# Optimization experiments

Hardware: AMD Instinct MI355X
Metric: run time of the kernel (lower is better)

The kernel has to match this reference:

```python
import jax, jax.numpy as jnp
import numpy as np

K = 9                # snake kernel size
CENTER = K // 2
EXT = 1.0            # extend_scope
EPS = 1e-5           # GroupNorm eps (torch default)


def conv2d(x, w, b, stride, padding):
    out = jax.lax.conv_general_dilated(
        x, w, window_strides=stride, padding=padding,
        dimension_numbers=("NCHW", "OIHW", "NCHW"))
    return out + b[None, :, None, None]


def group_norm(x, gamma, beta, groups):
    B, C, H, W = x.shape
    xg = x.reshape(B, groups, C // groups, H, W)
    mu = xg.mean(axis=(2, 3, 4), keepdims=True)
    var = xg.var(axis=(2, 3, 4), keepdims=True)
    xn = ((xg - mu) / jnp.sqrt(var + EPS)).reshape(B, C, H, W)
    return xn * gamma[None, :, None, None] + beta[None, :, None, None]


def setup_inputs() -> dict:
    key = jax.random.key(0)
    ks = jax.random.split(key, 6)
    B, Cin, Cout, H, W = 4, 64, 64, 128, 128
    x = jax.random.normal(ks[0], (B, Cin, H, W), jnp.float32)
    w_off = jax.random.normal(ks[1], (2 * K, Cin, 3, 3), jnp.float32) * 0.05
    b_off = jax.random.normal(ks[2], (2 * K,), jnp.float32) * 0.01
    g_gn_off = jnp.ones((2 * K,), jnp.float32)
    b_gn_off = jnp.zeros((2 * K,), jnp.float32)
    w_dsc = jax.random.normal(ks[3], (Cout, Cin, K, 1), jnp.float32) * 0.05
    b_dsc = jax.random.normal(ks[4], (Cout,), jnp.float32) * 0.01
    g_gn = jnp.ones((Cout,), jnp.float32)
    b_gn = jnp.zeros((Cout,), jnp.float32)
    return {"x": x, "w_off": w_off, "b_off": b_off,
            "g_gn_off": g_gn_off, "b_gn_off": b_gn_off,
            "w_dsc": w_dsc, "b_dsc": b_dsc, "g_gn": g_gn, "b_gn": b_gn}


def reference(x, w_off, b_off, g_gn_off, b_gn_off, w_dsc, b_dsc, g_gn, b_gn):
    B, Cin, H, W = x.shape
    # offset branch: conv3x3 -> GN(K groups over 2K chans) -> tanh
    off = conv2d(x, w_off, b_off, (1, 1), "SAME")
    off = jnp.tanh(group_norm(off, g_gn_off, b_gn_off, K))
    y_off = off[:, :K]                              # morph=0 uses y offsets, [B,K,H,W]

    # cumulative offsets outward from the kernel center (center entry = 0)
    upper = jnp.cumsum(y_off[:, CENTER + 1:], axis=1)
    lower = jnp.flip(jnp.cumsum(jnp.flip(y_off[:, :CENTER], axis=1), axis=1), axis=1)
    y_off_new = jnp.concatenate(
        [lower, jnp.zeros_like(y_off[:, :1]), upper], axis=1)   # [B,K,H,W]

    # coordinate maps (pixel space)
    y_coord = jnp.arange(H, dtype=x.dtype)[None, None, :, None] + EXT * y_off_new
    x_spread = jnp.linspace(-CENTER, CENTER, K).astype(x.dtype)
    x_coord = jnp.broadcast_to(
        jnp.arange(W, dtype=x.dtype)[None, None, None, :]
        + x_spread[None, :, None, None], y_coord.shape)
    # rearrange b k h w -> b (h k) w
    y_map = y_coord.transpose(0, 2, 1, 3).reshape(B, H * K, W)
    x_map = x_coord.transpose(0, 2, 1, 3).reshape(B, H * K, W)

    # bilinear grid_sample, align_corners=True; clamp-to-range == torch's
    # _coordinate_map_scaling(clamp + [-1,1] normalize) then grid_sample
    yc = jnp.clip(y_map, 0.0, H - 1.0)
    xc = jnp.clip(x_map, 0.0, W - 1.0)
    y0 = jnp.floor(yc); x0 = jnp.floor(xc)
    wy = yc - y0; wx = xc - x0
    y0i = y0.astype(jnp.int32); x0i = x0.astype(jnp.int32)
    y1i = jnp.minimum(y0i + 1, H - 1); x1i = jnp.minimum(x0i + 1, W - 1)

    def samp(f, y0i, y1i, x0i, x1i, wy, wx):
        # f: [C,H,W]; indices/weights: [K*H, W] -> [C, K*H, W]
        v00 = f[:, y0i, x0i]; v01 = f[:, y0i, x1i]
        v10 = f[:, y1i, x0i]; v11 = f[:, y1i, x1i]
        return (v00 * (1 - wy) * (1 - wx) + v01 * (1 - wy) * wx
                + v10 * wy * (1 - wx) + v11 * wy * wx)

    deformed = jax.vmap(samp)(x, y0i, y1i, x0i, x1i, wy, wx)  # [B,C,K*H,W]

    # snake conv: kernel (K,1), stride (K,1), then GN(out//4) + ReLU
    out = conv2d(deformed, w_dsc, b_dsc, (K, 1), "VALID")      # [B,Cout,H,W]
    out = group_norm(out, g_gn, b_gn, w_dsc.shape[0] // 4)
    return jax.nn.relu(out)
```

## Files before the change

### kernel.cpp

```cpp
#include <hip/hip_runtime.h>
#include <hip/hip_bf16.h>
#include <math.h>

#define B 4
#define C 64
#define H 128
#define W 128
#define KK 9
#define CENTER 4
#define HW (H*W)
#define HP 130
#define WP 130

typedef __attribute__((ext_vector_type(8))) short short8;
typedef __attribute__((ext_vector_type(4))) float f4;

#define OFF_OFFT   0
#define OFF_XB     786432
#define OFF_WB     2949632
#define OFF_WOB    2968064
#define OFF_CSUM   2972672
#define OFF_OSUM   2980864

__device__ __forceinline__ unsigned bf16pack(float a, float b) {
    unsigned ua = __builtin_bit_cast(unsigned, a) + 0x8000u;
    unsigned ub = __builtin_bit_cast(unsigned, b) + 0x8000u;
    return __builtin_amdgcn_perm(ub, ua, 0x07060302);
}

__device__ __forceinline__ unsigned lerp_pack(unsigned a, unsigned b, float fw) {
    float alo = __builtin_bit_cast(float, a << 16);
    float ahi = __builtin_bit_cast(float, a & 0xffff0000u);
    float blo = __builtin_bit_cast(float, b << 16);
    float bhi = __builtin_bit_cast(float, b & 0xffff0000u);
    float slo = alo + fw * (blo - alo);
    float shi = ahi + fw * (bhi - ahi);
    return bf16pack(slo, shi);
}

__device__ __forceinline__ float fast_tanh(float x) {
    float e = __expf(2.f * x);
    return 1.f - 2.f * __builtin_amdgcn_rcpf(e + 1.f);
}

__global__ __launch_bounds__(256) void k_prep(const float* __restrict__ x,
                                              const float* __restrict__ w_dsc,
                                              const float* __restrict__ w_off,
                                              unsigned short* __restrict__ xb,
                                              unsigned short* __restrict__ wb,
                                              unsigned short* __restrict__ wob,
                                              float* __restrict__ csum) {
    int bid = blockIdx.x;
    int tid = threadIdx.x;
    if (bid < 2048) {
        __shared__ float lt[64 * 33];
        int xcd = bid & 7, i = bid >> 3;
        int c = i & 3, hc = (i >> 2) & 15, b = i >> 6;
        int h = (xcd << 4) | hc;
        int w0 = c * 32;
        int ciA = tid >> 2, gA = tid & 3;
        int wlB = tid >> 3, cgB = tid & 7;

        if (c == 0 && tid < 8)
            *(uint4*)(xb + ((size_t)(b * HP + h + 1) * WP) * 64 + tid * 8)
                = make_uint4(0, 0, 0, 0);
        if (c == 3 && tid < 8)
            *(uint4*)(xb + (((size_t)(b * HP + h + 1) * WP) + WP - 1) * 64 + tid * 8)
                = make_uint4(0, 0, 0, 0);
        {
            const float* src = x + ((size_t)(b * C + ciA) * HW) + h * W + w0 + gA * 8;
            float4 v0 = *(const float4*)src;
            float4 v1 = *(const float4*)(src + 4);
            float* d = lt + ciA * 33 + gA * 8;
            d[0] = v0.x; d[1] = v0.y; d[2] = v0.z; d[3] = v0.w;
            d[4] = v1.x; d[5] = v1.y; d[6] = v1.z; d[7] = v1.w;
        }
        __syncthreads();
        {
            unsigned u[4];
#pragma unroll
            for (int i2 = 0; i2 < 4; i2++) {
                float lo = lt[(cgB * 8 + 2 * i2)     * 33 + wlB];
                float hi = lt[(cgB * 8 + 2 * i2 + 1) * 33 + wlB];
                u[i2] = bf16pack(lo, hi);
            }
            *(uint4*)(xb + ((size_t)((b * HP + h + 1) * WP + w0 + wlB + 1)) * 64 + cgB * 8) =
                make_uint4(u[0], u[1], u[2], u[3]);
        }
    } else if (bid < 2048 + 8) {
        int r = bid - 2048;
        int b = r >> 1, which = r & 1;
        unsigned short* dst = xb + ((size_t)(b * HP + which * (HP - 1)) * WP) * 64;
        for (int t = tid; t < WP * 64 / 8; t += 256)
            *(uint4*)(dst + t * 8) = make_uint4(0, 0, 0, 0);
    } else if (bid < 2048 + 8 + 180) {
        int idx = (bid - (2048 + 8)) * 256 + tid;
        if (idx < KK * C * C) {
            int k  = idx >> 12;
            int r  = idx & 4095;
            int co = r >> 6;
            int ci = r & 63;
            unsigned u = __builtin_bit_cast(unsigned, w_dsc[(co * C + ci) * KK + k]);
            u = (u + 0x7fffu + ((u >> 16) & 1u)) >> 16;
            wb[idx] = (unsigned short)u;
        } else if (idx < KK * C * C + 9 * 16 * 64) {
            int r   = idx - KK * C * C;
            int tap = r >> 10;
            int j   = (r >> 6) & 15;
            int ci  = r & 63;
            float v = (j < 10) ? w_off[(j * C + ci) * 9 + tap] : 0.f;
            unsigned u = __builtin_bit_cast(unsigned, v);
            u = (u + 0x7fffu + ((u >> 16) & 1u)) >> 16;
            wob[r] = (unsigned short)u;
        }
    } else {
        int z = bid - (2048 + 8 + 180);
        int base = z * 1024 + tid * 4;
        *(f4*)(csum + base) = 0;
    }
}

__global__ __launch_bounds__(256, 4) void k_offconv(const unsigned short* __restrict__ xb,
                                                    const unsigned short* __restrict__ wob,
                                                    const float* __restrict__ b_off,
                                                    float* __restrict__ offT,
                                                    float* __restrict__ osum16) {
    __shared__ float red[80];
    int bid = blockIdx.x;
    int xcd  = bid & 7;
    int i    = bid >> 3;
    int b    = i >> 5;
    int rest = i & 31;
    int h    = (xcd << 4) | (rest >> 1);
    int half = rest & 1;
    int tid  = threadIdx.x;
    int wid  = tid >> 6;
    int lane = tid & 63;
    int lm = lane & 15, qd = lane >> 4;
    int pw = half * 64 + wid * 16;

    f4 acc = 0;
    const unsigned short* xrow = xb + ((size_t)(b * HP + h) * WP) * 64;
#pragma unroll
    for (int s = 0; s < 2; s++) {
        int co_ofs = s * 32 + qd * 8;
        short8 a_[9], w_[9];
#pragma unroll
        for (int t = 0; t < 9; t++) {
            int ky = t / 3, kx = t - 3 * (t / 3);
            a_[t] = *(const short8*)(xrow +
                ((size_t)(ky * WP + pw + lm + kx)) * 64 + co_ofs);
            w_[t] = *(const short8*)(wob + (t * 16 + lm) * 64 + co_ofs);
        }
#pragma unroll
        for (int t = 0; t < 9; t++)
            acc = __builtin_amdgcn_mfma_f32_16x16x32_bf16(a_[t], w_[t], acc, 0, 0, 0);
    }

    float bo = b_off[lm];
    float sv = 0.f, sq = 0.f;
    int pixbase = (b * H + h) * W;
#pragma unroll
    for (int r = 0; r < 4; r++) {
        float val = acc[r] + bo;
        int p = pw + qd * 4 + r;
        if (lm < 10) {
            offT[(size_t)(pixbase + p) * 12 + lm] = val;
            sv += val; sq += val * val;
        }
    }
    sv += __shfl_xor(sv, 16); sv += __shfl_xor(sv, 32);
    sq += __shfl_xor(sq, 16); sq += __shfl_xor(sq, 32);
    if (lane < 16 && lm < 10) {
        red[(wid * 10 + lm) * 2]     = sv;
        red[(wid * 10 + lm) * 2 + 1] = sq;
    }
    __syncthreads();
    if (tid < 20) {
        int j = tid >> 1, comp = tid & 1;
        float s = red[j * 2 + comp] + red[(10 + j) * 2 + comp] +
                  red[(20 + j) * 2 + comp] + red[(30 + j) * 2 + comp];
        int sidx = (h >> 3) & 15;
        atomicAdd(&osum16[sidx * 40 + b * 10 + (j >> 1) * 2 + comp], s);
    }
}

__global__ __launch_bounds__(256, 4) void k_main(const unsigned short* __restrict__ xb,
                                                 const float* __restrict__ offT,
                                                 const float* __restrict__ osum16,
                                                 const float* __restrict__ g_gn_off,
                                                 const float* __restrict__ b_gn_off,
                                                 const unsigned short* __restrict__ wb,
                                                 const float* __restrict__ b_dsc,
                                                 float* __restrict__ outp,
                                                 float* __restrict__ csum16) {
    __shared__ float red[512];
    __shared__ float sred[16];

    int bid = blockIdx.x;
    int xcd  = bid & 7;
    int i    = bid >> 3;
    int b    = i >> 5;
    int rest = i & 31;
    int h    = (xcd << 4) | (rest >> 1);
    int p0   = (rest & 1) << 6;
    int tid  = threadIdx.x;
    int wid  = tid >> 6;
    int lane = tid & 63;
    int lm = lane & 15, qd = lane >> 4;

    int ps = p0 + wid * 16 + lm;

    if (tid < 160) {
        int gc = tid >> 4, s = tid & 15;
        float v = osum16[s * 40 + b * 10 + gc];
        v += __shfl_xor(v, 1); v += __shfl_xor(v, 2);
        v += __shfl_xor(v, 4); v += __shfl_xor(v, 8);
        if (s == 0) sred[gc] = v;
    }
    __syncthreads();

    float yoff[KK];
    {
        const float inv_n = 1.f / (2.f * HW);
        const float* op = offT + (size_t)((b * H + h) * W + ps) * 12;
        f4 o0 = *(const f4*)op;
        f4 o1 = *(const f4*)(op + 4);
        float o8 = op[8];
        float raw[KK] = {o0[0], o0[1], o0[2], o0[3], o1[0], o1[1], o1[2], o1[3], o8};
        float v[KK];
#pragma unroll
        for (int j = 0; j < KK; j++) {
            int g = j >> 1;
            float s  = sred[g * 2];
            float s2 = sred[g * 2 + 1];
            float mean = s * inv_n;
            float var  = s2 * inv_n - mean * mean;
            float rstd = rsqrtf(var + 1e-5f);
            v[j] = fast_tanh((raw[j] - mean) * rstd * g_gn_off[j] + b_gn_off[j]);
        }
        yoff[CENTER] = 0.f;
        float run = 0.f;
#pragma unroll
        for (int k = CENTER - 1; k >= 0; k--) { run += v[k]; yoff[k] = run; }
        run = 0.f;
#pragma unroll
        for (int k = CENTER + 1; k < KK; k++) { run += v[k]; yoff[k] = run; }
    }

    f4 acc[4];
#pragma unroll
    for (int ct = 0; ct < 4; ct++) acc[ct] = 0;

#pragma unroll
    for (int kg = 0; kg < 3; kg++) {
        int   ofsA[3], ofsB[3];
        float fw[3];
#pragma unroll
        for (int j = 0; j < 3; j++) {
            int k = kg * 3 + j;
            float yc = fminf(fmaxf((float)h + yoff[k], 0.f), (float)(H - 1));
            float fy = floorf(yc);
            int y0 = (int)fy;
            int dy = (y0 < H - 1) ? (WP * 64) : 0;
            fw[j] = yc - fy;
            int xi = min(max(ps + k - CENTER, 0), W - 1);
            ofsA[j] = ((b * HP + y0 + 1) * WP + xi + 1) * 64 + qd * 8;
            ofsB[j] = ofsA[j] + dy;
        }
#pragma unroll
        for (int s = 0; s < 2; s++) {
            int so = s * 32;
            uint4 ga[3], gb[3];
#pragma unroll
            for (int j = 0; j < 3; j++) {
                ga[j] = *(const uint4*)(xb + ofsA[j] + so);
                gb[j] = *(const uint4*)(xb + ofsB[j] + so);
            }
#pragma unroll
            for (int j = 0; j < 3; j++) {
                int k = kg * 3 + j;
                const unsigned short* wk = wb + k * (C * C);
                uint4 r;
                r.x = lerp_pack(ga[j].x, gb[j].x, fw[j]);
                r.y = lerp_pack(ga[j].y, gb[j].y, fw[j]);
                r.z = lerp_pack(ga[j].z, gb[j].z, fw[j]);
                r.w = lerp_pack(ga[j].w, gb[j].w, fw[j]);
                short8 afr = __builtin_bit_cast(short8, r);
#pragma unroll
                for (int ct = 0; ct < 4; ct++) {
                    short8 bfr = *(const short8*)(wk + (ct * 16 + lm) * 64 +
                                                  so + qd * 8);
                    acc[ct] = __builtin_amdgcn_mfma_f32_16x16x32_bf16(afr, bfr,
                                                                      acc[ct], 0, 0, 0);
                }
            }
        }
    }

#pragma unroll
    for (int ct = 0; ct < 4; ct++) {
        int co = ct * 16 + lm;
        float bias = b_dsc[co];
        f4 v;
        float sv = 0.f, sq = 0.f;
#pragma unroll
        for (int r = 0; r < 4; r++) {
            v[r] = acc[ct][r] + bias;
            sv += v[r]; sq += v[r] * v[r];
        }
        *(f4*)(outp + ((size_t)(b * C + co)) * HW + h * W + p0 + wid * 16 + qd * 4) = v;
        sv += __shfl_xor(sv, 16); sv += __shfl_xor(sv, 32);
        sq += __shfl_xor(sq, 16); sq += __shfl_xor(sq, 32);
        if (lane < 16) {
            red[((wid * 4 + ct) * 16 + lm) * 2]     = sv;
            red[((wid * 4 + ct) * 16 + lm) * 2 + 1] = sq;
        }
    }
    __syncthreads();
    if (tid < 128) {
        int co = tid >> 1, comp = tid & 1;
        int ct = co >> 4, lmr = co & 15;
        float s = 0.f;
#pragma unroll
        for (int w2 = 0; w2 < 4; w2++)
            s += red[((w2 * 4 + ct) * 16 + lmr) * 2 + comp];
        int sidx = (h >> 3) & 15;
        atomicAdd(&csum16[(sidx * 256 + b * 64 + co) * 2 + comp], s);
    }
}

__global__ __launch_bounds__(256) void k_norm(float* __restrict__ outp,
                                              const float* __restrict__ csum16,
                                              const float* __restrict__ g_gn,
                                              const float* __restrict__ b_gn) {
    __shared__ float lds[128];
    int bid = blockIdx.x;
    int xcd = bid & 7;
    int i   = bid >> 3;
    int bc  = i >> 1;
    int c2  = (xcd << 1) | (i & 1);
    int b = bc >> 6, co = bc & 63;
    int grp = co >> 2;
    int tid = threadIdx.x;

    if (tid < 128) {
        int s = tid >> 3, c = (tid >> 1) & 3, comp = tid & 1;
        lds[tid] = csum16[(s * 256 + b * 64 + grp * 4 + c) * 2 + comp];
    }
    __syncthreads();
#pragma unroll
    for (int st = 64; st >= 2; st >>= 1) {
        if (tid < st) lds[tid] += lds[tid + st];
        __syncthreads();
    }
    float S = lds[0], S2 = lds[1];
    float n = 4.f * HW;
    float mean = S / n;
    float var  = S2 / n - mean * mean;
    float rstd = rsqrtf(var + 1e-5f);
    float sc = rstd * g_gn[co];
    float sh = b_gn[co] - mean * sc;

    int idx = (bc * 16 + c2) * 256 + tid;
    float4* ptr = (float4*)outp;
    float4 vv = ptr[idx];
    vv.x = fmaxf(vv.x * sc + sh, 0.f);
    vv.y = fmaxf(vv.y * sc + sh, 0.f);
    vv.z = fmaxf(vv.z * sc + sh, 0.f);
    vv.w = fmaxf(vv.w * sc + sh, 0.f);
    ptr[idx] = vv;
}

extern "C" void kernel_launch(void* const* d_in, const int* in_sizes, int n_in,
                              void* d_out, int out_size, void* d_ws, size_t ws_size,
                              hipStream_t stream) {
    const float* x        = (const float*)d_in[0];
    const float* w_off    = (const float*)d_in[1];
    const float* b_off    = (const float*)d_in[2];
    const float* g_gn_off = (const float*)d_in[3];
    const float* b_gn_off = (const float*)d_in[4];
    const float* w_dsc    = (const float*)d_in[5];
    const float* b_dsc    = (const float*)d_in[6];
    const float* g_gn     = (const float*)d_in[7];
    const float* b_gn     = (const float*)d_in[8];
    float* out = (float*)d_out;
    float* ws  = (float*)d_ws;

    float*          offT   = ws + OFF_OFFT;
    unsigned short* xbp    = (unsigned short*)(ws + OFF_XB);
    unsigned short* wbp    = (unsigned short*)(ws + OFF_WB);
    unsigned short* wobp   = (unsigned short*)(ws + OFF_WOB);
    float*          csum16 = ws + OFF_CSUM;
    float*          osum16 = ws + OFF_OSUM;

    k_prep<<<2048 + 8 + 180 + 9, 256, 0, stream>>>(x, w_dsc, w_off, xbp, wbp,
                                                   wobp, csum16);
    k_offconv<<<2 * B * H, 256, 0, stream>>>(xbp, wobp, b_off, offT, osum16);
    k_main<<<2 * B * H, 256, 0, stream>>>(xbp, offT, osum16, g_gn_off, b_gn_off,
                                          wbp, b_dsc, out, csum16);
    k_norm<<<B * C * HW / 4 / 256, 256, 0, stream>>>(out, csum16, g_gn, b_gn);
}
```

Before: 166.9 us.

## Stage conv weights in swizzled LDS for offset conv and snake conv

Both kernels now copy their bf16 weight fragments from global memory into XOR-swizzled shared memory, and the MFMA B operands are read from LDS instead of global. In the main kernel the weights are loaded in two channel halves, so the K-loop is reordered into two passes (s=0, then s=1) with a barrier and reload between them. The aim is to cut repeated global and L2 weight traffic and avoid LDS bank conflicts. The cost is extra shared memory, around 36 KB in the main kernel, which may limit occupancy, plus added synchronization.

```diff
diff --git a/kernel.cpp b/kernel.cpp
--- a/kernel.cpp
+++ b/kernel.cpp
@@ -125,6 +125,7 @@
                                                     const float* __restrict__ b_off,
                                                     float* __restrict__ offT,
                                                     float* __restrict__ osum16) {
+    __shared__ unsigned short wlds[1152 * 8];
     __shared__ float red[80];
     int bid = blockIdx.x;
     int xcd  = bid & 7;
@@ -139,22 +140,33 @@
     int lm = lane & 15, qd = lane >> 4;
     int pw = half * 64 + wid * 16;
 
+    for (int c = tid; c < 1152; c += 256) {
+        int row = c >> 3, g = c & 7;
+        uint4 v = *(const uint4*)(wob + c * 8);
+        int dst = (g ^ (row & 7)) * 144 + row;
+        *(uint4*)(wlds + dst * 8) = v;
+    }
+    __syncthreads();
+
     f4 acc = 0;
     const unsigned short* xrow = xb + ((size_t)(b * HP + h) * WP) * 64;
 #pragma unroll
     for (int s = 0; s < 2; s++) {
         int co_ofs = s * 32 + qd * 8;
-        short8 a_[9], w_[9];
+        short8 a_[9];
 #pragma unroll
         for (int t = 0; t < 9; t++) {
             int ky = t / 3, kx = t - 3 * (t / 3);
             a_[t] = *(const short8*)(xrow +
                 ((size_t)(ky * WP + pw + lm + kx)) * 64 + co_ofs);
-            w_[t] = *(const short8*)(wob + (t * 16 + lm) * 64 + co_ofs);
-        }
-#pragma unroll
-        for (int t = 0; t < 9; t++)
-            acc = __builtin_amdgcn_mfma_f32_16x16x32_bf16(a_[t], w_[t], acc, 0, 0, 0);
+        }
+#pragma unroll
+        for (int t = 0; t < 9; t++) {
+            int row = t * 16 + lm;
+            int chunk = (((s * 4 + qd) ^ (lm & 7)) * 144) + row;
+            short8 w = *(const short8*)(wlds + chunk * 8);
+            acc = __builtin_amdgcn_mfma_f32_16x16x32_bf16(a_[t], w, acc, 0, 0, 0);
+        }
     }
 
     float bo = b_off[lm];
@@ -194,6 +206,7 @@
                                                  const float* __restrict__ b_dsc,
                                                  float* __restrict__ outp,
                                                  float* __restrict__ csum16) {
+    __shared__ unsigned short wlds[2304 * 8];
     __shared__ float red[512];
     __shared__ float sred[16];
 
@@ -218,6 +231,12 @@
         v += __shfl_xor(v, 4); v += __shfl_xor(v, 8);
         if (s == 0) sred[gc] = v;
     }
+    for (int c = tid; c < 2304; c += 256) {
+        int k = c >> 8, row = (c >> 2) & 63, g2 = c & 3;
+        uint4 v = *(const uint4*)(wb + (size_t)k * 4096 + row * 64 + g2 * 8);
+        int dst = ((g2 ^ (row & 3)) * 576) + k * 64 + row;
+        *(uint4*)(wlds + dst * 8) = v;
+    }
     __syncthreads();
 
     float yoff[KK];
@@ -252,35 +271,33 @@
 #pragma unroll
     for (int ct = 0; ct < 4; ct++) acc[ct] = 0;
 
-#pragma unroll
-    for (int kg = 0; kg < 3; kg++) {
-        int   ofsA[3], ofsB[3];
-        float fw[3];
-#pragma unroll
-        for (int j = 0; j < 3; j++) {
-            int k = kg * 3 + j;
-            float yc = fminf(fmaxf((float)h + yoff[k], 0.f), (float)(H - 1));
-            float fy = floorf(yc);
-            int y0 = (int)fy;
-            int dy = (y0 < H - 1) ? (WP * 64) : 0;
-            fw[j] = yc - fy;
-            int xi = min(max(ps + k - CENTER, 0), W - 1);
-            ofsA[j] = ((b * HP + y0 + 1) * WP + xi + 1) * 64 + qd * 8;
-            ofsB[j] = ofsA[j] + dy;
-        }
-#pragma unroll
-        for (int s = 0; s < 2; s++) {
-            int so = s * 32;
-            uint4 ga[3], gb[3];
-#pragma unroll
-            for (int j = 0; j < 3; j++) {
-                ga[j] = *(const uint4*)(xb + ofsA[j] + so);
-                gb[j] = *(const uint4*)(xb + ofsB[j] + so);
-            }
+    auto kpass = [&](int s) {
+        int so = s * 32;
+#pragma unroll
+        for (int kg = 0; kg < 3; kg++) {
+            int   ofsA[3], ofsB[3];
+            float fw[3];
 #pragma unroll
             for (int j = 0; j < 3; j++) {
                 int k = kg * 3 + j;
-                const unsigned short* wk = wb + k * (C * C);
+                float yc = fminf(fmaxf((float)h + yoff[k], 0.f), (float)(H - 1));
+                float fy = floorf(yc);
+                int y0 = (int)fy;
+                int dy = (y0 < H - 1) ? (WP * 64) : 0;
+                fw[j] = yc - fy;
+                int xi = min(max(ps + k - CENTER, 0), W - 1);
+                ofsA[j] = ((b * HP + y0 + 1) * WP + xi + 1) * 64 + qd * 8 + so;
+                ofsB[j] = ofsA[j] + dy;
+            }
+            uint4 ga[3], gb[3];
+#pragma unroll
+            for (int j = 0; j < 3; j++) {
+                ga[j] = *(const uint4*)(xb + ofsA[j]);
+                gb[j] = *(const uint4*)(xb + ofsB[j]);
+            }
+#pragma unroll
+            for (int j = 0; j < 3; j++) {
+                int k = kg * 3 + j;
                 uint4 r;
                 r.x = lerp_pack(ga[j].x, gb[j].x, fw[j]);
                 r.y = lerp_pack(ga[j].y, gb[j].y, fw[j]);
@@ -289,14 +306,26 @@
                 short8 afr = __builtin_bit_cast(short8, r);
 #pragma unroll
                 for (int ct = 0; ct < 4; ct++) {
-                    short8 bfr = *(const short8*)(wk + (ct * 16 + lm) * 64 +
-                                                  so + qd * 8);
+                    int row = ct * 16 + lm;
+                    int chunk = ((qd ^ (lm & 3)) * 576) + k * 64 + row;
+                    short8 bfr = *(const short8*)(wlds + chunk * 8);
                     acc[ct] = __builtin_amdgcn_mfma_f32_16x16x32_bf16(afr, bfr,
                                                                       acc[ct], 0, 0, 0);
                 }
             }
         }
-    }
+    };
+
+    kpass(0);
+    __syncthreads();
+    for (int c = tid; c < 2304; c += 256) {
+        int k = c >> 8, row = (c >> 2) & 63, g2 = c & 3;
+        uint4 v = *(const uint4*)(wb + (size_t)k * 4096 + row * 64 + (4 + g2) * 8);
+        int dst = ((g2 ^ (row & 3)) * 576) + k * 64 + row;
+        *(uint4*)(wlds + dst * 8) = v;
+    }
+    __syncthreads();
+    kpass(1);
 
 #pragma unroll
     for (int ct = 0; ct < 4; ct++) {
```

Result: faster. 134.9 us, median of 3 (-19.2%).
